# Performance work log

Measured on AMD Instinct MI355X. Metric: run time of the kernel, lower is better.

The kernel has to match this reference:

```python
import jax, jax.numpy as jnp
import numpy as np

B, T, IN, H, L, P = 512, 512, 1, 100, 4, 0.5  # batch, seq, input, hidden, layers, dropout


def setup_inputs() -> dict:
    key = jax.random.key(0)
    ks = jax.random.split(key, 12)
    k = 1.0 / np.sqrt(H)  # torch nn.LSTM init scale
    u = lambda kk, shape: jax.random.uniform(kk, shape, jnp.float32, -k, k)
    inp = {
        "x": jax.random.normal(ks[0], (B, T, IN), jnp.float32),
        "W_ih0": u(ks[1], (4 * H, IN)),          # layer 0 input weights
        "W_ih_rest": u(ks[2], (L - 1, 4 * H, H)),  # layers 1..3 input weights
        "W_hh": u(ks[3], (L, 4 * H, H)),
        "b_ih": u(ks[4], (L, 4 * H)),
        "b_hh": u(ks[5], (L, 4 * H)),
        "W_out": u(ks[6], (1, H)),
        "b_out": u(ks[7], (1,)),
        # inter-layer dropout keep-masks (torch applies dropout to outputs of layers 0..L-2)
        "drop_masks": jax.random.bernoulli(ks[8], 1.0 - P, (L - 1, B, T, H)).astype(jnp.float32),
    }
    return inp


def _lstm_layer(seq, Wih, Whh, b):
    # seq: [T, B, in_dim]; returns [T, B, H]. PyTorch gate order: i, f, g, o.
    h0 = jnp.zeros((seq.shape[1], Whh.shape[-1]), seq.dtype)

    def step(carry, xt):
        h, c = carry
        gates = xt @ Wih.T + h @ Whh.T + b  # [B, 4H]
        i, f, g, o = jnp.split(gates, 4, axis=-1)
        c = jax.nn.sigmoid(f) * c + jax.nn.sigmoid(i) * jnp.tanh(g)
        h = jax.nn.sigmoid(o) * jnp.tanh(c)
        return (h, c), h

    _, hs = jax.lax.scan(step, (h0, h0), seq)
    return hs


def reference(x, W_ih0, W_ih_rest, W_hh, b_ih, b_hh, W_out, b_out, drop_masks):
    scale = 1.0 / (1.0 - P)
    seq = jnp.swapaxes(x, 0, 1)  # [T, B, IN] (batch_first -> time-major)
    seq = _lstm_layer(seq, W_ih0, W_hh[0], b_ih[0] + b_hh[0])
    for l in range(1, L):
        seq = seq * (jnp.swapaxes(drop_masks[l - 1], 0, 1) * scale)
        seq = _lstm_layer(seq, W_ih_rest[l - 1], W_hh[l], b_ih[l] + b_hh[l])
    last = seq[-1]  # [B, H] == lstm_out[:, -1]
    return last @ W_out.T + b_out  # [B, 1]
```

## Files before the change

### kernel.cpp

```cpp
#include <hip/hip_runtime.h>
#include <cstdint>
#include <cstddef>

#define BB 512
#define TT 512
#define HH 100
#define G4 400

template<bool IS_L0, bool WRITE_DROP>
__global__ __launch_bounds__(448, 2)
void rec_kernel(const float* __restrict__ x,
                const float* __restrict__ xc,
                const float* __restrict__ Whh_l,
                const float* __restrict__ Wih0,
                const float* __restrict__ bih_l,
                const float* __restrict__ bhh_l,
                const float* __restrict__ dmask_l,
                float* __restrict__ hdrop,
                float* __restrict__ st_h,
                float* __restrict__ st_c)
{
    __shared__ float hbuf[2][2][112];
    __shared__ float gsh[2][400];

    const int tid = threadIdx.x;
    const bool rowok = tid < G4;
    const int row = rowok ? tid : (G4 - 1);
    const int b0 = blockIdx.x * 2;
    const int b1 = b0 + 1;

    float wf[100];
    {
        const float4* ws4 = (const float4*)(Whh_l + (size_t)row * HH);
        #pragma unroll
        for (int m = 0; m < 25; ++m) ((float4*)wf)[m] = ws4[m];
    }

    float wx = 0.f, bs = 0.f;
    if (IS_L0) { wx = Wih0[row]; bs = bih_l[row] + bhh_l[row]; }

    ((float*)hbuf)[tid] = 0.f;

    const bool p2 = (tid < HH) || (tid >= 256 && tid < 256 + HH);
    const int e2 = (tid >= 256) ? 1 : 0;
    const int jj = (tid >= 256) ? (tid - 256) : tid;
    const int be = b0 + e2;
    float c2 = 0.f, hlast = 0.f;

    __syncthreads();

    float gin0 = 0.f, gin1 = 0.f, xv0 = 0.f, xv1 = 0.f, mk = 0.f;
    if (IS_L0) {
        xv0 = x[(size_t)b0 * TT];
        xv1 = x[(size_t)b1 * TT];
    } else {
        gin0 = xc[(size_t)b0 * G4 + row];
        gin1 = xc[(size_t)b1 * G4 + row];
    }
    if (WRITE_DROP && p2) mk = dmask_l[(size_t)be * TT * HH + jj];

    int cur = 0;
    for (int t = 0; t < TT; ++t) {
        const int tn = (t + 1 < TT) ? (t + 1) : t;

        float nxv0 = 0.f, nxv1 = 0.f, ngin0 = 0.f, ngin1 = 0.f, nmk = 0.f;
        if (IS_L0) {
            nxv0 = x[(size_t)b0 * TT + tn];
            nxv1 = x[(size_t)b1 * TT + tn];
        } else {
            const size_t base = (size_t)tn * BB * G4;
            ngin0 = xc[base + (size_t)b0 * G4 + row];
            ngin1 = xc[base + (size_t)b1 * G4 + row];
        }
        if (WRITE_DROP && p2) nmk = dmask_l[((size_t)be * TT + tn) * HH + jj];

        if (IS_L0) {
            gin0 = fmaf(xv0, wx, bs);
            gin1 = fmaf(xv1, wx, bs);
        }

        float s0a = 0.f, s0b = 0.f, s1a = 0.f, s1b = 0.f;
        const float4* h0p = (const float4*)&hbuf[cur][0][0];
        const float4* h1p = (const float4*)&hbuf[cur][1][0];
        #pragma unroll
        for (int p = 0; p < 25; ++p) {
            const float4 a = h0p[p];
            const float4 b = h1p[p];
            s0a = fmaf(wf[4 * p + 0], a.x, s0a);
            s0b = fmaf(wf[4 * p + 1], a.y, s0b);
            s0a = fmaf(wf[4 * p + 2], a.z, s0a);
            s0b = fmaf(wf[4 * p + 3], a.w, s0b);
            s1a = fmaf(wf[4 * p + 0], b.x, s1a);
            s1b = fmaf(wf[4 * p + 1], b.y, s1b);
            s1a = fmaf(wf[4 * p + 2], b.z, s1a);
            s1b = fmaf(wf[4 * p + 3], b.w, s1b);
        }
        if (rowok) {
            gsh[0][row] = s0a + s0b + gin0;
            gsh[1][row] = s1a + s1b + gin1;
        }
        __syncthreads();

        const int nxt = cur ^ 1;
        if (p2) {
            const float gi = gsh[e2][jj];
            const float gf = gsh[e2][HH + jj];
            const float gg = gsh[e2][2 * HH + jj];
            const float go = gsh[e2][3 * HH + jj];
            const float i_ = 1.f / (1.f + __expf(-gi));
            const float f_ = 1.f / (1.f + __expf(-gf));
            const float o_ = 1.f / (1.f + __expf(-go));
            const float gt = 1.f - 2.f / (__expf(gg + gg) + 1.f);
            c2 = fmaf(f_, c2, i_ * gt);
            const float th = 1.f - 2.f / (__expf(c2 + c2) + 1.f);
            const float h = o_ * th;
            hlast = h;
            hbuf[nxt][e2][jj] = h;
            if (WRITE_DROP)
                hdrop[((size_t)t * BB + be) * HH + jj] = h * mk * 2.f;
        }
        __syncthreads();
        cur = nxt;
        gin0 = ngin0; gin1 = ngin1;
        xv0 = nxv0;   xv1 = nxv1;
        mk = nmk;
    }

    if (p2) {
        st_h[(size_t)be * HH + jj] = hlast;
        st_c[(size_t)be * HH + jj] = c2;
    }
}

__global__ __launch_bounds__(256, 2)
void xc_gemm(const float* __restrict__ A,
             const float* __restrict__ W,
             const float* __restrict__ bih_l,
             const float* __restrict__ bhh_l,
             float* __restrict__ xc)
{
    __shared__ float At[HH][132];
    __shared__ float Bt[HH][68];

    const int tid = threadIdx.x;
    const int n0  = blockIdx.x * 64;
    const size_t m0 = (size_t)blockIdx.y * 128;

    for (int s = tid; s < 128 * 25; s += 256) {
        const int r = s / 25, kq = s - r * 25;
        const float4 v = *(const float4*)&A[(m0 + r) * HH + kq * 4];
        At[kq * 4 + 0][r] = v.x; At[kq * 4 + 1][r] = v.y;
        At[kq * 4 + 2][r] = v.z; At[kq * 4 + 3][r] = v.w;
    }
    for (int s = tid; s < 64 * 25; s += 256) {
        const int r = s / 25, kq = s - r * 25;
        const int col = n0 + r;
        float4 v = {0.f, 0.f, 0.f, 0.f};
        if (col < G4) v = *(const float4*)&W[(size_t)col * HH + kq * 4];
        Bt[kq * 4 + 0][r] = v.x; Bt[kq * 4 + 1][r] = v.y;
        Bt[kq * 4 + 2][r] = v.z; Bt[kq * 4 + 3][r] = v.w;
    }
    __syncthreads();

    const int tx = tid & 15;
    const int ty = tid >> 4;
    float acc[8][4];
    #pragma unroll
    for (int i = 0; i < 8; ++i)
        #pragma unroll
        for (int j = 0; j < 4; ++j) acc[i][j] = 0.f;

    #pragma unroll 4
    for (int k = 0; k < HH; ++k) {
        const float4 a0 = *(const float4*)&At[k][ty * 8];
        const float4 a1 = *(const float4*)&At[k][ty * 8 + 4];
        const float4 bv = *(const float4*)&Bt[k][tx * 4];
        const float av[8] = {a0.x, a0.y, a0.z, a0.w, a1.x, a1.y, a1.z, a1.w};
        #pragma unroll
        for (int i = 0; i < 8; ++i) {
            acc[i][0] = fmaf(av[i], bv.x, acc[i][0]);
            acc[i][1] = fmaf(av[i], bv.y, acc[i][1]);
            acc[i][2] = fmaf(av[i], bv.z, acc[i][2]);
            acc[i][3] = fmaf(av[i], bv.w, acc[i][3]);
        }
    }

    const int col = n0 + tx * 4;
    if (col < G4) {
        const float4 u = *(const float4*)&bih_l[col];
        const float4 v = *(const float4*)&bhh_l[col];
        const float4 bias = {u.x + v.x, u.y + v.y, u.z + v.z, u.w + v.w};
        #pragma unroll
        for (int i = 0; i < 8; ++i) {
            const size_t r = m0 + ty * 8 + i;
            float4 o = {acc[i][0] + bias.x, acc[i][1] + bias.y,
                        acc[i][2] + bias.z, acc[i][3] + bias.w};
            *(float4*)&xc[r * G4 + col] = o;
        }
    }
}

__global__ __launch_bounds__(256)
void out_kernel(const float* __restrict__ st_h3,
                const float* __restrict__ Wout,
                const float* __restrict__ bout,
                float* __restrict__ out)
{
    const int b = blockIdx.x * 256 + threadIdx.x;
    if (b < BB) {
        float sum = bout[0];
        #pragma unroll 4
        for (int k = 0; k < HH; ++k)
            sum = fmaf(st_h3[(size_t)b * HH + k], Wout[k], sum);
        out[b] = sum;
    }
}

extern "C" void kernel_launch(void* const* d_in, const int* in_sizes, int n_in,
                              void* d_out, int out_size, void* d_ws, size_t ws_size,
                              hipStream_t stream)
{
    const float* x     = (const float*)d_in[0];
    const float* Wih0  = (const float*)d_in[1];
    const float* WihR  = (const float*)d_in[2];
    const float* Whh   = (const float*)d_in[3];
    const float* bih   = (const float*)d_in[4];
    const float* bhh   = (const float*)d_in[5];
    const float* Wout  = (const float*)d_in[6];
    const float* bout  = (const float*)d_in[7];
    const float* dmask = (const float*)d_in[8];
    float* out = (float*)d_out;

    float* ws    = (float*)d_ws;
    float* xcb   = ws;
    float* hdrop = xcb + (size_t)TT * BB * G4;
    float* sth   = hdrop + (size_t)TT * BB * HH;
    float* stc   = sth + (size_t)4 * BB * HH;

    const dim3 rgrid(BB / 2), rblk(448);
    const dim3 ggrid(7, (TT * BB) / 128), gblk(256);

    rec_kernel<true, true><<<rgrid, rblk, 0, stream>>>(
        x, nullptr, Whh, Wih0, bih, bhh, dmask,
        hdrop, sth, stc);
    for (int l = 1; l < 4; ++l) {
        xc_gemm<<<ggrid, gblk, 0, stream>>>(
            hdrop, WihR + (size_t)(l - 1) * G4 * HH,
            bih + l * G4, bhh + l * G4, xcb);
        if (l < 3) {
            rec_kernel<false, true><<<rgrid, rblk, 0, stream>>>(
                nullptr, xcb, Whh + (size_t)l * G4 * HH,
                nullptr, nullptr, nullptr,
                dmask + (size_t)l * BB * TT * HH,
                hdrop, sth + (size_t)l * BB * HH, stc + (size_t)l * BB * HH);
        } else {
            rec_kernel<false, false><<<rgrid, rblk, 0, stream>>>(
                nullptr, xcb, Whh + (size_t)l * G4 * HH,
                nullptr, nullptr, nullptr,
                nullptr,
                nullptr, sth + (size_t)l * BB * HH, stc + (size_t)l * BB * HH);
        }
    }
    out_kernel<<<dim3(2), dim3(256), 0, stream>>>(sth + (size_t)3 * BB * HH, Wout, bout, out);
}
```

Before: 4.406 ms.

## Remap recurrent threads to two gate rows for one batch element each

Each thread now holds two rows of W_hh in registers (rows p and p+200) and computes them for a single batch element chosen by the low bit of the thread index. Previously each thread held one row and computed it for both batch elements. The change halves the LDS reads of h per FMA pair, since both batch-element threads read different h vectors, and lets one warp cover both batch elements in the gate phase. The cost is doubled weight register pressure (200 floats per thread) at a 448-thread, 2-blocks launch bound, which risks spills or lower occupancy.

```diff
diff --git a/kernel.cpp b/kernel.cpp
--- a/kernel.cpp
+++ b/kernel.cpp
@@ -24,89 +24,95 @@
     __shared__ float gsh[2][400];
 
     const int tid = threadIdx.x;
-    const bool rowok = tid < G4;
-    const int row = rowok ? tid : (G4 - 1);
-    const int b0 = blockIdx.x * 2;
-    const int b1 = b0 + 1;
-
-    float wf[100];
+    const int p   = tid >> 1;
+    const int e   = tid & 1;
+    const bool rowok = (p < 200);
+    const int pc  = rowok ? p : 199;
+    const int r0  = pc;
+    const int r1  = pc + 200;
+    const int b   = blockIdx.x * 2 + e;
+
+    float wf0[100], wf1[100];
     {
-        const float4* ws4 = (const float4*)(Whh_l + (size_t)row * HH);
-        #pragma unroll
-        for (int m = 0; m < 25; ++m) ((float4*)wf)[m] = ws4[m];
-    }
-
-    float wx = 0.f, bs = 0.f;
-    if (IS_L0) { wx = Wih0[row]; bs = bih_l[row] + bhh_l[row]; }
+        const float4* w0 = (const float4*)(Whh_l + (size_t)r0 * HH);
+        const float4* w1 = (const float4*)(Whh_l + (size_t)r1 * HH);
+        #pragma unroll
+        for (int m = 0; m < 25; ++m) {
+            ((float4*)wf0)[m] = w0[m];
+            ((float4*)wf1)[m] = w1[m];
+        }
+    }
+
+    float wx0 = 0.f, wx1 = 0.f, bs0 = 0.f, bs1 = 0.f;
+    if (IS_L0) {
+        wx0 = Wih0[r0];  bs0 = bih_l[r0] + bhh_l[r0];
+        wx1 = Wih0[r1];  bs1 = bih_l[r1] + bhh_l[r1];
+    }
 
     ((float*)hbuf)[tid] = 0.f;
 
-    const bool p2 = (tid < HH) || (tid >= 256 && tid < 256 + HH);
-    const int e2 = (tid >= 256) ? 1 : 0;
-    const int jj = (tid >= 256) ? (tid - 256) : tid;
-    const int be = b0 + e2;
+    const bool p2 = (p < HH);
+    const int jj  = p2 ? p : 0;
     float c2 = 0.f, hlast = 0.f;
 
     __syncthreads();
 
-    float gin0 = 0.f, gin1 = 0.f, xv0 = 0.f, xv1 = 0.f, mk = 0.f;
+    float gin0 = 0.f, gin1 = 0.f, xv = 0.f, mk = 0.f;
     if (IS_L0) {
-        xv0 = x[(size_t)b0 * TT];
-        xv1 = x[(size_t)b1 * TT];
+        xv = x[(size_t)b * TT];
     } else {
-        gin0 = xc[(size_t)b0 * G4 + row];
-        gin1 = xc[(size_t)b1 * G4 + row];
-    }
-    if (WRITE_DROP && p2) mk = dmask_l[(size_t)be * TT * HH + jj];
+        gin0 = xc[(size_t)b * G4 + r0];
+        gin1 = xc[(size_t)b * G4 + r1];
+    }
+    if (WRITE_DROP && p2) mk = dmask_l[(size_t)b * TT * HH + jj];
 
     int cur = 0;
     for (int t = 0; t < TT; ++t) {
         const int tn = (t + 1 < TT) ? (t + 1) : t;
 
-        float nxv0 = 0.f, nxv1 = 0.f, ngin0 = 0.f, ngin1 = 0.f, nmk = 0.f;
+        float nxv = 0.f, ngin0 = 0.f, ngin1 = 0.f, nmk = 0.f;
         if (IS_L0) {
-            nxv0 = x[(size_t)b0 * TT + tn];
-            nxv1 = x[(size_t)b1 * TT + tn];
+            nxv = x[(size_t)b * TT + tn];
         } else {
-            const size_t base = (size_t)tn * BB * G4;
-            ngin0 = xc[base + (size_t)b0 * G4 + row];
-            ngin1 = xc[base + (size_t)b1 * G4 + row];
-        }
-        if (WRITE_DROP && p2) nmk = dmask_l[((size_t)be * TT + tn) * HH + jj];
+            const size_t base = (size_t)tn * BB * G4 + (size_t)b * G4;
+            ngin0 = xc[base + r0];
+            ngin1 = xc[base + r1];
+        }
+        if (WRITE_DROP && p2) nmk = dmask_l[((size_t)b * TT + tn) * HH + jj];
 
         if (IS_L0) {
-            gin0 = fmaf(xv0, wx, bs);
-            gin1 = fmaf(xv1, wx, bs);
-        }
-
-        float s0a = 0.f, s0b = 0.f, s1a = 0.f, s1b = 0.f;
-        const float4* h0p = (const float4*)&hbuf[cur][0][0];
-        const float4* h1p = (const float4*)&hbuf[cur][1][0];
-        #pragma unroll
-        for (int p = 0; p < 25; ++p) {
-            const float4 a = h0p[p];
-            const float4 b = h1p[p];
-            s0a = fmaf(wf[4 * p + 0], a.x, s0a);
-            s0b = fmaf(wf[4 * p + 1], a.y, s0b);
-            s0a = fmaf(wf[4 * p + 2], a.z, s0a);
-            s0b = fmaf(wf[4 * p + 3], a.w, s0b);
-            s1a = fmaf(wf[4 * p + 0], b.x, s1a);
-            s1b = fmaf(wf[4 * p + 1], b.y, s1b);
-            s1a = fmaf(wf[4 * p + 2], b.z, s1a);
-            s1b = fmaf(wf[4 * p + 3], b.w, s1b);
+            gin0 = fmaf(xv, wx0, bs0);
+            gin1 = fmaf(xv, wx1, bs1);
+        }
+
+        float a0 = 0.f, a0b = 0.f, a1 = 0.f, a1b = 0.f;
+        {
+            const float4* hp = (const float4*)&hbuf[cur][e][0];
+            #pragma unroll
+            for (int m = 0; m < 25; ++m) {
+                const float4 hv = hp[m];
+                a0  = fmaf(wf0[4 * m + 0], hv.x, a0);
+                a0b = fmaf(wf0[4 * m + 1], hv.y, a0b);
+                a0  = fmaf(wf0[4 * m + 2], hv.z, a0);
+                a0b = fmaf(wf0[4 * m + 3], hv.w, a0b);
+                a1  = fmaf(wf1[4 * m + 0], hv.x, a1);
+                a1b = fmaf(wf1[4 * m + 1], hv.y, a1b);
+                a1  = fmaf(wf1[4 * m + 2], hv.z, a1);
+                a1b = fmaf(wf1[4 * m + 3], hv.w, a1b);
+            }
         }
         if (rowok) {
-            gsh[0][row] = s0a + s0b + gin0;
-            gsh[1][row] = s1a + s1b + gin1;
+            gsh[e][pc]       = a0 + a0b + gin0;
+            gsh[e][pc + 200] = a1 + a1b + gin1;
         }
         __syncthreads();
 
         const int nxt = cur ^ 1;
         if (p2) {
-            const float gi = gsh[e2][jj];
-            const float gf = gsh[e2][HH + jj];
-            const float gg = gsh[e2][2 * HH + jj];
-            const float go = gsh[e2][3 * HH + jj];
+            const float gi = gsh[e][jj];
+            const float gf = gsh[e][HH + jj];
+            const float gg = gsh[e][2 * HH + jj];
+            const float go = gsh[e][3 * HH + jj];
             const float i_ = 1.f / (1.f + __expf(-gi));
             const float f_ = 1.f / (1.f + __expf(-gf));
             const float o_ = 1.f / (1.f + __expf(-go));
@@ -115,20 +121,19 @@
             const float th = 1.f - 2.f / (__expf(c2 + c2) + 1.f);
             const float h = o_ * th;
             hlast = h;
-            hbuf[nxt][e2][jj] = h;
+            hbuf[nxt][e][jj] = h;
             if (WRITE_DROP)
-                hdrop[((size_t)t * BB + be) * HH + jj] = h * mk * 2.f;
+                hdrop[((size_t)t * BB + b) * HH + jj] = h * mk * 2.f;
         }
         __syncthreads();
         cur = nxt;
         gin0 = ngin0; gin1 = ngin1;
-        xv0 = nxv0;   xv1 = nxv1;
-        mk = nmk;
+        xv = nxv; mk = nmk;
     }
 
     if (p2) {
-        st_h[(size_t)be * HH + jj] = hlast;
-        st_c[(size_t)be * HH + jj] = c2;
+        st_h[(size_t)b * HH + jj] = hlast;
+        st_c[(size_t)b * HH + jj] = c2;
     }
 }
 
```

Result: faster. 4.155 ms (-5.7%).
